# Kernel tuning notes

Measured on AMD Instinct MI355X. Metric: run time of the kernel, lower is better.

The kernel has to match this reference:

```python
import jax, jax.numpy as jnp
import numpy as np

IN_FEATURES = 4096
OUT_FEATURES = 16384
TOKENS = 32


def setup_inputs() -> dict:
    key = jax.random.key(0)
    k1, k2, k3, k4 = jax.random.split(key, 4)
    x = jax.random.normal(k1, (TOKENS, IN_FEATURES), dtype=jnp.float16)
    # int8-valued weights in [-127, 127]
    weight_int8 = jax.random.randint(k2, (OUT_FEATURES, IN_FEATURES), -127, 128, dtype=jnp.int32)
    # per-output-channel scale, positive (amax/127 in the original)
    scale = (jax.random.uniform(k3, (OUT_FEATURES,), dtype=jnp.float32) * 0.02 + 1e-4).astype(jnp.float16)
    bias = jax.random.normal(k4, (OUT_FEATURES,), dtype=jnp.float16)
    return {"x": x, "weight_int8": weight_int8, "scale": scale, "bias": bias}


def reference(x, weight_int8, scale, bias):
    # Dequantize int8 weights to compute dtype with per-row scale, then linear.
    w = weight_int8.astype(jnp.float16) * scale[:, None]          # [out, in] fp16
    return jnp.dot(x, w.T) + bias                                  # [tokens, out]
```

## Files before the change

kernel.cpp:

```cpp
#include <hip/hip_runtime.h>
#include <hip/hip_bf16.h>


typedef __attribute__((ext_vector_type(4))) int    i32x4;
typedef __attribute__((ext_vector_type(4))) float  f32x4;
typedef __attribute__((ext_vector_type(8))) short  s16x8;
typedef __attribute__((ext_vector_type(8))) __bf16 bf16x8;

constexpr int K = 4096;
constexpr int N = 16384;
constexpr int T = 32;
constexpr int KSPLIT = 4;
constexpr int KPW = K / KSPLIT;
constexpr size_t XB_OFF = 0;
constexpr size_t PART_OFF = 262144;

__device__ inline unsigned short f2bf_rne(float f) {
    unsigned u = __builtin_bit_cast(unsigned, f);
    u += 0x7FFF + ((u >> 16) & 1);
    return (unsigned short)(u >> 16);
}

__device__ inline bf16x8 cvtW(i32x4 lo, i32x4 hi) {
    s16x8 r;
#pragma unroll
    for (int i = 0; i < 4; ++i) {
        r[i]     = (short)(__builtin_bit_cast(unsigned, (float)lo[i]) >> 16);
        r[i + 4] = (short)(__builtin_bit_cast(unsigned, (float)hi[i]) >> 16);
    }
    return __builtin_bit_cast(bf16x8, r);
}

__global__ __launch_bounds__(256) void xcvt_kernel(const float* __restrict__ x,
                                                   unsigned short* __restrict__ xb) {
    const int i = (blockIdx.x * 256 + threadIdx.x) * 8;
    f32x4 lo = *reinterpret_cast<const f32x4*>(x + i);
    f32x4 hi = *reinterpret_cast<const f32x4*>(x + i + 4);
    s16x8 r;
#pragma unroll
    for (int j = 0; j < 4; ++j) {
        r[j]     = (short)f2bf_rne(lo[j]);
        r[j + 4] = (short)f2bf_rne(hi[j]);
    }
    *reinterpret_cast<s16x8*>(xb + i) = r;
}

__global__ __launch_bounds__(256, 4) void w8gemm_kernel(
    const __bf16* __restrict__ xb,
    const int* __restrict__ w,
    float* __restrict__ partial)
{
    const int lane = threadIdx.x & 63;
    const int wave = threadIdx.x >> 6;
    const int n16  = lane & 15;
    const int quad = lane >> 4;

    const int g  = blockIdx.x & 255;
    const int ks = blockIdx.x >> 8;

    const int c = g * 64 + wave * 16 + n16;
    const int k0 = ks * KPW;

    const int*   __restrict__ wrow = w + (size_t)c * K + k0;
    const __bf16* __restrict__ xr0 = xb + (size_t)n16 * K + k0;
    const __bf16* __restrict__ xr1 = xb + (size_t)(n16 + 16) * K + k0;

    f32x4 acc0 = {0.f, 0.f, 0.f, 0.f};
    f32x4 acc1 = {0.f, 0.f, 0.f, 0.f};

    i32x4 bA[4], bB[4];
    bf16x8 aA[4], aB[4];

    auto load_chunk = [&](int kc, i32x4* bb, bf16x8* aa) {
        const int e0 = kc + quad * 8;
        const int e1 = e0 + 32;
        bb[0] = *reinterpret_cast<const i32x4*>(wrow + e0);
        bb[1] = *reinterpret_cast<const i32x4*>(wrow + e0 + 4);
        bb[2] = *reinterpret_cast<const i32x4*>(wrow + e1);
        bb[3] = *reinterpret_cast<const i32x4*>(wrow + e1 + 4);
        aa[0] = *reinterpret_cast<const bf16x8*>(xr0 + e0);
        aa[1] = *reinterpret_cast<const bf16x8*>(xr1 + e0);
        aa[2] = *reinterpret_cast<const bf16x8*>(xr0 + e1);
        aa[3] = *reinterpret_cast<const bf16x8*>(xr1 + e1);
    };
    auto compute_chunk = [&](const i32x4* bb, const bf16x8* aa) {
        bf16x8 bf0 = cvtW(bb[0], bb[1]);
        acc0 = __builtin_amdgcn_mfma_f32_16x16x32_bf16(aa[0], bf0, acc0, 0, 0, 0);
        acc1 = __builtin_amdgcn_mfma_f32_16x16x32_bf16(aa[1], bf0, acc1, 0, 0, 0);
        bf16x8 bf1 = cvtW(bb[2], bb[3]);
        acc0 = __builtin_amdgcn_mfma_f32_16x16x32_bf16(aa[2], bf1, acc0, 0, 0, 0);
        acc1 = __builtin_amdgcn_mfma_f32_16x16x32_bf16(aa[3], bf1, acc1, 0, 0, 0);
    };

    load_chunk(0, bA, aA);
#pragma unroll 1
    for (int kc = 0; kc < KPW; kc += 128) {
        load_chunk(kc + 64, bB, aB);
        compute_chunk(bA, aA);
        if (kc + 128 < KPW) load_chunk(kc + 128, bA, aA);
        compute_chunk(bB, aB);
    }

    float* __restrict__ p = partial + (size_t)ks * T * N;
#pragma unroll
    for (int v = 0; v < 4; ++v) {
        const int row = quad * 4 + v;
        p[(size_t)row * N + c]        = acc0[v];
        p[(size_t)(row + 16) * N + c] = acc1[v];
    }
}

__global__ __launch_bounds__(256) void reduce_kernel(
    const float* __restrict__ partial,
    const float* __restrict__ scale,
    const float* __restrict__ bias,
    float* __restrict__ out)
{
    const int i = (blockIdx.x * 256 + threadIdx.x) * 4;
    const int c = i & (N - 1);
    f32x4 s = *reinterpret_cast<const f32x4*>(partial + i);
#pragma unroll
    for (int ks = 1; ks < KSPLIT; ++ks) {
        f32x4 pv = *reinterpret_cast<const f32x4*>(partial + (size_t)ks * T * N + i);
        s[0] += pv[0]; s[1] += pv[1]; s[2] += pv[2]; s[3] += pv[3];
    }
    f32x4 sc = *reinterpret_cast<const f32x4*>(scale + c);
    f32x4 bi = *reinterpret_cast<const f32x4*>(bias + c);
    f32x4 r = {s[0] * sc[0] + bi[0], s[1] * sc[1] + bi[1],
               s[2] * sc[2] + bi[2], s[3] * sc[3] + bi[3]};
    *reinterpret_cast<f32x4*>(out + i) = r;
}

extern "C" void kernel_launch(void* const* d_in, const int* in_sizes, int n_in,
                              void* d_out, int out_size, void* d_ws, size_t ws_size,
                              hipStream_t stream) {
    const float* x     = (const float*)d_in[0];
    const int*   w     = (const int*)d_in[1];
    const float* scale = (const float*)d_in[2];
    const float* bias  = (const float*)d_in[3];
    float* out = (float*)d_out;

    unsigned short* xb = (unsigned short*)((char*)d_ws + XB_OFF);
    float* part        = (float*)((char*)d_ws + PART_OFF);

    xcvt_kernel<<<dim3(64), dim3(256), 0, stream>>>(x, xb);
    w8gemm_kernel<<<dim3(256 * KSPLIT), dim3(256), 0, stream>>>(
        (const __bf16*)xb, w, part);
    reduce_kernel<<<dim3((T * N / 4) / 256), dim3(256), 0, stream>>>(
        part, scale, bias, out);
}
```

Measured before the change: 389.1 us.

## Stage int8 weights through LDS via direct global-to-LDS loads, halve K-split

Replaces the per-lane register prefetch of weight rows with wave-wide global_load_lds transfers. Each wave's 16 weight rows go into padded LDS tiles of 256 K-elements, which lanes then read back in MFMA layout. Halving KSPLIT from 4 to 2 also cuts partial-sum traffic and reduction work, at the cost of fewer blocks. The single LDS buffer has no double buffering, and the syncs around it may expose load latency.

```diff
diff --git a/kernel.cpp b/kernel.cpp
--- a/kernel.cpp
+++ b/kernel.cpp
@@ -10,8 +10,11 @@
 constexpr int K = 4096;
 constexpr int N = 16384;
 constexpr int T = 32;
-constexpr int KSPLIT = 4;
+constexpr int KSPLIT = 2;
 constexpr int KPW = K / KSPLIT;
+constexpr int BK = 256;
+constexpr int NT = KPW / BK;
+constexpr int ROWPITCH = 1024 + 16;
 constexpr size_t XB_OFF = 0;
 constexpr size_t PART_OFF = 262144;
 
@@ -45,11 +48,13 @@
     *reinterpret_cast<s16x8*>(xb + i) = r;
 }
 
-__global__ __launch_bounds__(256, 4) void w8gemm_kernel(
+__global__ __launch_bounds__(256, 2) void w8gemm_kernel(
     const __bf16* __restrict__ xb,
     const int* __restrict__ w,
     float* __restrict__ partial)
 {
+    extern __shared__ char smem[];
+
     const int lane = threadIdx.x & 63;
     const int wave = threadIdx.x >> 6;
     const int n16  = lane & 15;
@@ -57,50 +62,55 @@
 
     const int g  = blockIdx.x & 255;
     const int ks = blockIdx.x >> 8;
+    const int kbase = ks * KPW;
 
-    const int c = g * 64 + wave * 16 + n16;
-    const int k0 = ks * KPW;
+    const char* gW0 = (const char*)w
+        + ((size_t)(g * 64 + wave * 16) * K + kbase) * 4 + (size_t)lane * 16;
+    char* lds0 = smem + (wave * 16) * ROWPITCH + lane * 16;
 
-    const int*   __restrict__ wrow = w + (size_t)c * K + k0;
-    const __bf16* __restrict__ xr0 = xb + (size_t)n16 * K + k0;
-    const __bf16* __restrict__ xr1 = xb + (size_t)(n16 + 16) * K + k0;
+    auto stage = [&](int it) {
+        const char* gp = gW0 + (size_t)it * BK * 4;
+#pragma unroll
+        for (int j = 0; j < 16; ++j) {
+            __builtin_amdgcn_global_load_lds(
+                (const __attribute__((address_space(1))) void*)(gp + (size_t)j * K * 4),
+                (__attribute__((address_space(3))) void*)(lds0 + j * ROWPITCH),
+                16, 0, 0);
+        }
+    };
+
+    const __bf16* __restrict__ xr0 = xb + (size_t)n16 * K + kbase + quad * 8;
+    const __bf16* __restrict__ xr1 = xr0 + (size_t)16 * K;
 
     f32x4 acc0 = {0.f, 0.f, 0.f, 0.f};
     f32x4 acc1 = {0.f, 0.f, 0.f, 0.f};
 
-    i32x4 bA[4], bB[4];
-    bf16x8 aA[4], aB[4];
+    const char* lrow = smem + (wave * 16 + n16) * ROWPITCH + quad * 32;
 
-    auto load_chunk = [&](int kc, i32x4* bb, bf16x8* aa) {
-        const int e0 = kc + quad * 8;
-        const int e1 = e0 + 32;
-        bb[0] = *reinterpret_cast<const i32x4*>(wrow + e0);
-        bb[1] = *reinterpret_cast<const i32x4*>(wrow + e0 + 4);
-        bb[2] = *reinterpret_cast<const i32x4*>(wrow + e1);
-        bb[3] = *reinterpret_cast<const i32x4*>(wrow + e1 + 4);
-        aa[0] = *reinterpret_cast<const bf16x8*>(xr0 + e0);
-        aa[1] = *reinterpret_cast<const bf16x8*>(xr1 + e0);
-        aa[2] = *reinterpret_cast<const bf16x8*>(xr0 + e1);
-        aa[3] = *reinterpret_cast<const bf16x8*>(xr1 + e1);
-    };
-    auto compute_chunk = [&](const i32x4* bb, const bf16x8* aa) {
-        bf16x8 bf0 = cvtW(bb[0], bb[1]);
-        acc0 = __builtin_amdgcn_mfma_f32_16x16x32_bf16(aa[0], bf0, acc0, 0, 0, 0);
-        acc1 = __builtin_amdgcn_mfma_f32_16x16x32_bf16(aa[1], bf0, acc1, 0, 0, 0);
-        bf16x8 bf1 = cvtW(bb[2], bb[3]);
-        acc0 = __builtin_amdgcn_mfma_f32_16x16x32_bf16(aa[2], bf1, acc0, 0, 0, 0);
-        acc1 = __builtin_amdgcn_mfma_f32_16x16x32_bf16(aa[3], bf1, acc1, 0, 0, 0);
-    };
-
-    load_chunk(0, bA, aA);
+    stage(0);
 #pragma unroll 1
-    for (int kc = 0; kc < KPW; kc += 128) {
-        load_chunk(kc + 64, bB, aB);
-        compute_chunk(bA, aA);
-        if (kc + 128 < KPW) load_chunk(kc + 128, bA, aA);
-        compute_chunk(bB, aB);
+    for (int it = 0; it < NT; ++it) {
+        bf16x8 aX0[8], aX1[8];
+#pragma unroll
+        for (int s = 0; s < 8; ++s) {
+            const int off = it * BK + s * 32;
+            aX0[s] = *reinterpret_cast<const bf16x8*>(xr0 + off);
+            aX1[s] = *reinterpret_cast<const bf16x8*>(xr1 + off);
+        }
+        __syncthreads();
+#pragma unroll
+        for (int s = 0; s < 8; ++s) {
+            i32x4 b0 = *reinterpret_cast<const i32x4*>(lrow + s * 128);
+            i32x4 b1 = *reinterpret_cast<const i32x4*>(lrow + s * 128 + 16);
+            bf16x8 bf = cvtW(b0, b1);
+            acc0 = __builtin_amdgcn_mfma_f32_16x16x32_bf16(aX0[s], bf, acc0, 0, 0, 0);
+            acc1 = __builtin_amdgcn_mfma_f32_16x16x32_bf16(aX1[s], bf, acc1, 0, 0, 0);
+        }
+        __syncthreads();
+        if (it + 1 < NT) stage(it + 1);
     }
 
+    const int c = g * 64 + wave * 16 + n16;
     float* __restrict__ p = partial + (size_t)ks * T * N;
 #pragma unroll
     for (int v = 0; v < 4; ++v) {
@@ -144,7 +154,7 @@
     float* part        = (float*)((char*)d_ws + PART_OFF);
 
     xcvt_kernel<<<dim3(64), dim3(256), 0, stream>>>(x, xb);
-    w8gemm_kernel<<<dim3(256 * KSPLIT), dim3(256), 0, stream>>>(
+    w8gemm_kernel<<<dim3(256 * KSPLIT), dim3(256), 64 * ROWPITCH, stream>>>(
         (const __bf16*)xb, w, part);
     reduce_kernel<<<dim3((T * N / 4) / 256), dim3(256), 0, stream>>>(
         part, scale, bias, out);
```

Result: no change. 383.2 us (-1.5%).
